# Kernel optimization log

Measured on AMD Instinct MI355X. Metric: run time of the kernel, lower is better.

## Reference

```python
import jax, jax.numpy as jnp
import numpy as np

B, T, C, H = 2, 2048, 1024, 16
D = C // H  # head_dim = 64
CH = C // 2


def _ln(x, g, b, eps=1e-5):
    m = x.mean(-1, keepdims=True)
    v = ((x - m) ** 2).mean(-1, keepdims=True)
    return (x - m) / jnp.sqrt(v + eps) * g + b


def setup_inputs() -> dict:
    key = jax.random.key(0)
    ks = iter(jax.random.split(key, 32))
    w = lambda shp: jax.random.normal(next(ks), shp, dtype=jnp.float32) * 0.02
    inp = {
        'x': jax.random.normal(next(ks), (B, T, C), dtype=jnp.float32),
        'attention_mask': jnp.ones((B, T, T), dtype=jnp.int32),
        # importance_net: Linear(C,C/2), LN(C/2), GELU, Linear(C/2,1), Sigmoid
        'imp_w1': w((C, CH)), 'imp_b1': jnp.zeros((CH,)),
        'imp_g': jnp.ones((CH,)), 'imp_beta': jnp.zeros((CH,)),
        'imp_w2': w((CH, 1)), 'imp_b2': jnp.zeros((1,)),
        # reasoning_net: Linear(C,C), LN(C), GELU, Linear(C,C)
        'rsn_w1': w((C, C)), 'rsn_b1': jnp.zeros((C,)),
        'rsn_g': jnp.ones((C,)), 'rsn_beta': jnp.zeros((C,)),
        'rsn_w2': w((C, C)), 'rsn_b2': jnp.zeros((C,)),
        # attention projections
        'q_w': w((C, C)), 'q_b': jnp.zeros((C,)),
        'k_w': w((C, C)), 'k_b': jnp.zeros((C,)),
        'v_w': w((C, C)), 'v_b': jnp.zeros((C,)),
        'o_w': w((C, C)), 'o_b': jnp.zeros((C,)),
        # temp_net: Linear(C,C/2), LN(C/2), GELU, Linear(C/2,H)
        'tmp_w1': w((C, CH)), 'tmp_b1': jnp.zeros((CH,)),
        'tmp_g': jnp.ones((CH,)), 'tmp_beta': jnp.zeros((CH,)),
        'tmp_w2': w((CH, H)), 'tmp_b2': jnp.zeros((H,)),
        # output LayerNorm
        'norm_g': jnp.ones((C,)), 'norm_b': jnp.zeros((C,)),
    }
    return inp


def reference(x, attention_mask, imp_w1, imp_b1, imp_g, imp_beta, imp_w2, imp_b2,
              rsn_w1, rsn_b1, rsn_g, rsn_beta, rsn_w2, rsn_b2,
              q_w, q_b, k_w, k_b, v_w, v_b, o_w, o_b,
              tmp_w1, tmp_b1, tmp_g, tmp_beta, tmp_w2, tmp_b2,
              norm_g, norm_b):
    Bz, Tz, Cz = x.shape
    # importance gating: [B,T,1]
    h = jax.nn.gelu(_ln(x @ imp_w1 + imp_b1, imp_g, imp_beta), approximate=False)
    importance = jnp.maximum(jax.nn.sigmoid(h @ imp_w2 + imp_b2), 1e-6)
    xi = x * importance
    # reasoning net on gated input
    h = jax.nn.gelu(_ln(xi @ rsn_w1 + rsn_b1, rsn_g, rsn_beta), approximate=False)
    reasoned = h @ rsn_w2 + rsn_b2
    # projections
    q = (reasoned @ q_w + q_b).reshape(Bz, Tz, H, D).transpose(0, 2, 1, 3)
    k = (xi @ k_w + k_b).reshape(Bz, Tz, H, D).transpose(0, 2, 1, 3)
    v = (x @ v_w + v_b).reshape(Bz, Tz, H, D).transpose(0, 2, 1, 3)
    # per-(batch,head) temperature
    ht = jax.nn.gelu(_ln(reasoned.mean(axis=1) @ tmp_w1 + tmp_b1, tmp_g, tmp_beta), approximate=False)
    temp = jax.nn.softplus(ht @ tmp_w2 + tmp_b2) + 0.5  # [B,H]
    # attention with mask and learned temperature before softmax
    scale = 1.0 / jnp.sqrt(jnp.float32(D))
    attn = jnp.einsum('bhqd,bhkd->bhqk', q, k) * scale
    attn = jnp.where(attention_mask[:, None] == 0, -jnp.inf, attn)
    attn = attn * temp[:, :, None, None]
    attn = jax.nn.softmax(attn, axis=-1)
    # dropout is identity in eval mode
    out = jnp.einsum('bhqk,bhkd->bhqd', attn, v)
    out = out.transpose(0, 2, 1, 3).reshape(Bz, Tz, Cz)
    out = out @ o_w + o_b
    return _ln(x + out, norm_g, norm_b)
```

## Files before the change

kernel.cpp:

```cpp
#include <hip/hip_runtime.h>
#include <hip/hip_bf16.h>
#include <math.h>

#define BB 2
#define TT 2048
#define CC 1024
#define HH 16
#define DD 64
#define CHALF 512
#define NN (BB * TT)
#define LOG2E 1.44269504088896340736f

typedef __attribute__((ext_vector_type(8))) short short8;
typedef __attribute__((ext_vector_type(4))) short short4_t;
typedef __attribute__((ext_vector_type(4))) float f32x4;

__device__ __forceinline__ float gelu_exact(float x) {
    return 0.5f * x * (1.0f + erff(x * 0.70710678118654752f));
}

__device__ __forceinline__ short f2bf(float f) {
    __hip_bfloat16 h = __float2bfloat16(f);
    short s;
    __builtin_memcpy(&s, &h, 2);
    return s;
}

__device__ __forceinline__ short4_t pack_bf16x4(float a, float b, float c,
                                                float d) {
    short4_t s4;
    s4[0] = f2bf(a);
    s4[1] = f2bf(b);
    s4[2] = f2bf(c);
    s4[3] = f2bf(d);
    return s4;
}

__device__ __forceinline__ void async_copy16(const void* g, void* l) {
    __builtin_amdgcn_global_load_lds(
        (const __attribute__((address_space(1))) void*)g,
        (__attribute__((address_space(3))) void*)l, 16, 0, 0);
}

__global__ __launch_bounds__(256) void prep(
    const float* __restrict__ x, __hip_bfloat16* __restrict__ x_bf,
    const int* __restrict__ mask, int* __restrict__ flags,
    const float* w0, const float* w1, const float* w2, const float* w3,
    const float* w4, const float* w5, const float* w6,
    __hip_bfloat16* t0, __hip_bfloat16* t1, __hip_bfloat16* t2,
    __hip_bfloat16* t3, __hip_bfloat16* t4, __hip_bfloat16* t5,
    __hip_bfloat16* t6) {
    __shared__ float T[64][65];
    int blk = blockIdx.x;
    int tid = threadIdx.x;
    if (blk < 2048) {
        int i = (blk * 256 + tid) * 8;
        float4 a = *(const float4*)&x[i];
        float4 b = *(const float4*)&x[i + 4];
        __hip_bfloat16 o[8] = {
            __float2bfloat16(a.x), __float2bfloat16(a.y),
            __float2bfloat16(a.z), __float2bfloat16(a.w),
            __float2bfloat16(b.x), __float2bfloat16(b.y),
            __float2bfloat16(b.z), __float2bfloat16(b.w)};
        *(float4*)&x_bf[i] = *(float4*)o;
    } else if (blk < 4096) {
        int idx = blk - 2048;
        int kt = idx & 31, qt = (idx >> 5) & 31, b = idx >> 10;
        int* red = (int*)T;
        int r = tid >> 2;
        int c0 = (tid & 3) * 16;
        const int* base =
            mask + ((size_t)(b * TT + qt * 64 + r)) * TT + kt * 64 + c0;
        int all = 1;
#pragma unroll
        for (int i = 0; i < 4; ++i) {
            int4 m4 = *(const int4*)(base + i * 4);
            all &= (m4.x != 0) & (m4.y != 0) & (m4.z != 0) & (m4.w != 0);
        }
        red[tid] = all;
        __syncthreads();
#pragma unroll
        for (int o = 128; o > 0; o >>= 1) {
            if (tid < o) red[tid] &= red[tid + o];
            __syncthreads();
        }
        if (tid == 0) flags[(b * 32 + qt) * 32 + kt] = red[0];
    } else {
        int idx = blk - 4096;
        const float* W;
        __hip_bfloat16* Wt;
        int N, n0, k0;
        if (idx < 128) {
            W = w0; Wt = t0; N = 512;
            n0 = (idx & 7) * 64;
            k0 = (idx >> 3) * 64;
        } else {
            idx -= 128;
            int w = idx >> 8;
            int r = idx & 255;
            N = 1024;
            n0 = (r & 15) * 64;
            k0 = (r >> 4) * 64;
            switch (w) {
                case 0: W = w1; Wt = t1; break;
                case 1: W = w2; Wt = t2; break;
                case 2: W = w3; Wt = t3; break;
                case 3: W = w4; Wt = t4; break;
                case 4: W = w5; Wt = t5; break;
                default: W = w6; Wt = t6; break;
            }
        }
        int c = tid & 63, r4 = tid >> 6;
#pragma unroll
        for (int i = 0; i < 16; ++i) {
            int row = i * 4 + r4;
            T[row][c] = W[(size_t)(k0 + row) * N + n0 + c];
        }
        __syncthreads();
#pragma unroll
        for (int i = 0; i < 16; ++i) {
            int row = i * 4 + r4;
            Wt[(size_t)(n0 + row) * CC + k0 + c] = __float2bfloat16(T[c][row]);
        }
    }
}

template <bool BF16OUT>
__global__ __launch_bounds__(256) void gemm_mfma64(
    const short* __restrict__ A, const short* __restrict__ Wt,
    const float* __restrict__ bias, float* __restrict__ Cf,
    __hip_bfloat16* __restrict__ Cb, int M, int N, int K) {
    __shared__ short As[64][32];
    __shared__ short Bs[128][32];
    int tid = threadIdx.x;
    int wave = tid >> 6, lane = tid & 63;
    int m16 = lane & 15, quad = lane >> 4;
    int wm = wave >> 1, wn = wave & 1;
    int row0 = blockIdx.y * 64, col0 = blockIdx.x * 128;
    int lr = lane >> 2;
    int kof = (lane & 3) * 8;

    f32x4 acc[2][4];
#pragma unroll
    for (int i = 0; i < 2; ++i)
#pragma unroll
        for (int j = 0; j < 4; ++j) acc[i][j] = (f32x4){0.f, 0.f, 0.f, 0.f};

    for (int k0 = 0; k0 < K; k0 += 32) {
        async_copy16(A + (size_t)(row0 + wave * 16 + lr) * K + k0 + kof,
                     &As[wave * 16][0]);
#pragma unroll
        for (int j = 0; j < 2; ++j) {
            int rbase = wave * 32 + j * 16;
            async_copy16(Wt + (size_t)(col0 + rbase + lr) * K + k0 + kof,
                         &Bs[rbase][0]);
        }
        __syncthreads();
        short8 af[2], bfr[4];
#pragma unroll
        for (int i = 0; i < 2; ++i)
            af[i] = *(const short8*)&As[wm * 32 + i * 16 + m16][quad * 8];
#pragma unroll
        for (int j = 0; j < 4; ++j)
            bfr[j] = *(const short8*)&Bs[wn * 64 + j * 16 + m16][quad * 8];
#pragma unroll
        for (int i = 0; i < 2; ++i)
#pragma unroll
            for (int j = 0; j < 4; ++j)
                acc[i][j] = __builtin_amdgcn_mfma_f32_16x16x32_bf16(
                    af[i], bfr[j], acc[i][j], 0, 0, 0);
        __syncthreads();
    }
#pragma unroll
    for (int i = 0; i < 2; ++i) {
#pragma unroll
        for (int j = 0; j < 4; ++j) {
            int col = col0 + wn * 64 + j * 16 + m16;
            float bv = bias[col];
#pragma unroll
            for (int rr = 0; rr < 4; ++rr) {
                int row = row0 + wm * 32 + i * 16 + quad * 4 + rr;
                float val = acc[i][j][rr] + bv;
                if (BF16OUT)
                    Cb[(size_t)row * N + col] = __float2bfloat16(val);
                else
                    Cf[(size_t)row * N + col] = val;
            }
        }
    }
}

__global__ __launch_bounds__(256) void gemm_qkv(
    const short* __restrict__ Aq, const short* __restrict__ Ak,
    const short* __restrict__ Av, const short* __restrict__ Wq,
    const short* __restrict__ Wk, const short* __restrict__ Wv,
    const float* __restrict__ bq, const float* __restrict__ bk,
    const float* __restrict__ bv, __hip_bfloat16* __restrict__ Cq,
    __hip_bfloat16* __restrict__ Ck, __hip_bfloat16* __restrict__ Cv,
    const float* __restrict__ tmp) {
    int z = blockIdx.z;
    const short* A = (z == 0) ? Aq : (z == 1) ? Ak : Av;
    const short* Wt = (z == 0) ? Wq : (z == 1) ? Wk : Wv;
    const float* bias = (z == 0) ? bq : (z == 1) ? bk : bv;

    __shared__ short As[128][32];
    __shared__ short Bs[128][32];
    int tid = threadIdx.x;
    int wave = tid >> 6, lane = tid & 63;
    int m16 = lane & 15, quad = lane >> 4;
    int wm = wave >> 1, wn = wave & 1;
    int row0 = blockIdx.y * 128, col0 = blockIdx.x * 128;
    int lr = lane >> 2;
    int kof = (lane & 3) * 8;

    float scale = 1.0f;
    if (z == 0)
        scale = tmp[(row0 >> 11) * HH + (col0 >> 6) + wn] * 0.125f * LOG2E;

    f32x4 acc[4][4];
#pragma unroll
    for (int i = 0; i < 4; ++i)
#pragma unroll
        for (int j = 0; j < 4; ++j) acc[i][j] = (f32x4){0.f, 0.f, 0.f, 0.f};

    for (int k0 = 0; k0 < CC; k0 += 32) {
#pragma unroll
        for (int j = 0; j < 2; ++j) {
            int rbase = wave * 32 + j * 16;
            async_copy16(A + (size_t)(row0 + rbase + lr) * CC + k0 + kof,
                         &As[rbase][0]);
            async_copy16(Wt + (size_t)(col0 + rbase + lr) * CC + k0 + kof,
                         &Bs[rbase][0]);
        }
        __syncthreads();
        short8 af[4], bfr[4];
#pragma unroll
        for (int i = 0; i < 4; ++i)
            af[i] = *(const short8*)&As[wm * 64 + i * 16 + m16][quad * 8];
#pragma unroll
        for (int j = 0; j < 4; ++j)
            bfr[j] = *(const short8*)&Bs[wn * 64 + j * 16 + m16][quad * 8];
#pragma unroll
        for (int i = 0; i < 4; ++i)
#pragma unroll
            for (int j = 0; j < 4; ++j)
                acc[i][j] = __builtin_amdgcn_mfma_f32_16x16x32_bf16(
                    af[i], bfr[j], acc[i][j], 0, 0, 0);
        __syncthreads();
    }
    if (z == 2) {
        int b = row0 >> 11;
        int t0r = (row0 & (TT - 1)) + wm * 64 + quad * 4;
#pragma unroll
        for (int i = 0; i < 4; ++i) {
#pragma unroll
            for (int j = 0; j < 4; ++j) {
                int col = col0 + wn * 64 + j * 16 + m16;
                int h = col >> 6, d = col & 63;
                float bv2 = bias[col];
                short4_t pk = pack_bf16x4(
                    acc[i][j][0] + bv2, acc[i][j][1] + bv2,
                    acc[i][j][2] + bv2, acc[i][j][3] + bv2);
                *(short4_t*)&Cv[(((size_t)(b * HH + h) * DD) + d) * TT + t0r +
                                i * 16] = pk;
            }
        }
    } else {
        __hip_bfloat16* C = (z == 0) ? Cq : Ck;
#pragma unroll
        for (int i = 0; i < 4; ++i) {
#pragma unroll
            for (int j = 0; j < 4; ++j) {
                int col = col0 + wn * 64 + j * 16 + m16;
                float bv2 = bias[col];
#pragma unroll
                for (int rr = 0; rr < 4; ++rr) {
                    int row = row0 + wm * 64 + i * 16 + quad * 4 + rr;
                    C[(size_t)row * CC + col] =
                        __float2bfloat16((acc[i][j][rr] + bv2) * scale);
                }
            }
        }
    }
}

__global__ __launch_bounds__(256) void imp_fused(
    const float* __restrict__ h1, const float* __restrict__ g,
    const float* __restrict__ beta, const float* __restrict__ w2,
    const float* __restrict__ b2, const float* __restrict__ x,
    __hip_bfloat16* __restrict__ xi) {
    int row = blockIdx.x;
    int tid = threadIdx.x;
    const float* hr = h1 + (size_t)row * CHALF;
    float v0 = hr[tid], v1 = hr[tid + 256];
    __shared__ float red[256];
    red[tid] = v0 + v1;
    __syncthreads();
#pragma unroll
    for (int o = 128; o > 0; o >>= 1) {
        if (tid < o) red[tid] += red[tid + o];
        __syncthreads();
    }
    float mean = red[0] * (1.0f / CHALF);
    __syncthreads();
    float d0 = v0 - mean, d1 = v1 - mean;
    red[tid] = d0 * d0 + d1 * d1;
    __syncthreads();
#pragma unroll
    for (int o = 128; o > 0; o >>= 1) {
        if (tid < o) red[tid] += red[tid + o];
        __syncthreads();
    }
    float inv = rsqrtf(red[0] * (1.0f / CHALF) + 1e-5f);
    __syncthreads();
    float ge0 = gelu_exact(d0 * inv * g[tid] + beta[tid]);
    float ge1 = gelu_exact(d1 * inv * g[tid + 256] + beta[tid + 256]);
    red[tid] = ge0 * w2[tid] + ge1 * w2[tid + 256];
    __syncthreads();
#pragma unroll
    for (int o = 128; o > 0; o >>= 1) {
        if (tid < o) red[tid] += red[tid + o];
        __syncthreads();
    }
    float z = red[0] + b2[0];
    float sg = 1.0f / (1.0f + expf(-z));
    float imp = fmaxf(sg, 1e-6f);
#pragma unroll
    for (int i = 0; i < 4; ++i) {
        int c = i * 256 + tid;
        xi[(size_t)row * CC + c] =
            __float2bfloat16(x[(size_t)row * CC + c] * imp);
    }
}

template <int WIDTH>
__global__ __launch_bounds__(256) void ln_gelu_bf16(
    const float* __restrict__ Y, const float* __restrict__ g,
    const float* __restrict__ beta, __hip_bfloat16* __restrict__ O) {
    constexpr int PT = WIDTH / 256;
    int row = blockIdx.x;
    int tid = threadIdx.x;
    const float* yr = Y + (size_t)row * WIDTH;
    float v[PT];
    float s = 0.f;
#pragma unroll
    for (int i = 0; i < PT; ++i) {
        v[i] = yr[i * 256 + tid];
        s += v[i];
    }
    __shared__ float red[256];
    red[tid] = s;
    __syncthreads();
#pragma unroll
    for (int o = 128; o > 0; o >>= 1) {
        if (tid < o) red[tid] += red[tid + o];
        __syncthreads();
    }
    float mean = red[0] * (1.0f / WIDTH);
    __syncthreads();
    s = 0.f;
#pragma unroll
    for (int i = 0; i < PT; ++i) {
        float d = v[i] - mean;
        s += d * d;
    }
    red[tid] = s;
    __syncthreads();
#pragma unroll
    for (int o = 128; o > 0; o >>= 1) {
        if (tid < o) red[tid] += red[tid + o];
        __syncthreads();
    }
    float inv = rsqrtf(red[0] * (1.0f / WIDTH) + 1e-5f);
#pragma unroll
    for (int i = 0; i < PT; ++i) {
        int c = i * 256 + tid;
        O[(size_t)row * WIDTH + c] =
            __float2bfloat16(gelu_exact((v[i] - mean) * inv * g[c] + beta[c]));
    }
}

__global__ __launch_bounds__(256) void mean_part(
    const __hip_bfloat16* __restrict__ R, float* __restrict__ part) {
    int idx = blockIdx.x * 256 + threadIdx.x;
    int c = idx & (CC - 1);
    int chunk = (idx >> 10) & 15;
    int b = idx >> 14;
    const __hip_bfloat16* base = R + ((size_t)(b * TT + chunk * 128)) * CC + c;
    float s = 0.f;
    for (int t = 0; t < 128; ++t) s += __bfloat162float(base[(size_t)t * CC]);
    part[idx] = s;
}

__global__ __launch_bounds__(256) void temp_gemv1(
    const float* __restrict__ part, const float* __restrict__ w1,
    const float* __restrict__ b1, float* __restrict__ acc1) {
    __shared__ float rm_l[CC];
    __shared__ float red[256];
    int b = blockIdx.y;
    int c0 = blockIdx.x * 64;
    int tid = threadIdx.x;
    for (int cc = tid; cc < CC; cc += 256) {
        float s = 0.f;
#pragma unroll
        for (int ch = 0; ch < 16; ++ch)
            s += part[(size_t)(b * 16 + ch) * CC + cc];
        rm_l[cc] = s * (1.0f / TT);
    }
    __syncthreads();
    int col = c0 + (tid & 63);
    int kq = tid >> 6;
    float s = 0.f;
#pragma unroll 8
    for (int i = kq * 256; i < kq * 256 + 256; ++i)
        s = fmaf(rm_l[i], w1[(size_t)i * CHALF + col], s);
    red[tid] = s;
    __syncthreads();
    if (tid < 64) {
        float t = red[tid] + red[tid + 64] + red[tid + 128] + red[tid + 192];
        acc1[b * CHALF + tid + c0] = t + b1[col];
    }
}

__global__ __launch_bounds__(512) void temp_fin(
    const float* __restrict__ acc1, const float* __restrict__ g,
    const float* __restrict__ beta, const float* __restrict__ w2,
    const float* __restrict__ b2, float* __restrict__ temp) {
    __shared__ float red[512];
    __shared__ float wred[8][16];
    int b = blockIdx.x;
    int tid = threadIdx.x;
    int wave = tid >> 6, lane = tid & 63;
    float acc = acc1[b * CHALF + tid];
    red[tid] = acc;
    __syncthreads();
#pragma unroll
    for (int o = 256; o > 0; o >>= 1) {
        if (tid < o) red[tid] += red[tid + o];
        __syncthreads();
    }
    float mean = red[0] * (1.0f / CHALF);
    __syncthreads();
    float d = acc - mean;
    red[tid] = d * d;
    __syncthreads();
#pragma unroll
    for (int o = 256; o > 0; o >>= 1) {
        if (tid < o) red[tid] += red[tid + o];
        __syncthreads();
    }
    float inv = rsqrtf(red[0] * (1.0f / CHALF) + 1e-5f);
    float ht = gelu_exact((acc - mean) * inv * g[tid] + beta[tid]);
    float p[16];
#pragma unroll
    for (int j = 0; j < 16; ++j) p[j] = ht * w2[tid * HH + j];
#pragma unroll
    for (int off = 1; off < 64; off <<= 1)
#pragma unroll
        for (int j = 0; j < 16; ++j) p[j] += __shfl_xor(p[j], off, 64);
    if (lane == 0)
#pragma unroll
        for (int j = 0; j < 16; ++j) wred[wave][j] = p[j];
    __syncthreads();
    if (tid < HH) {
        float s = b2[tid];
#pragma unroll
        for (int w = 0; w < 8; ++w) s += wred[w][tid];
        float sp = fmaxf(s, 0.f) + log1pf(expf(-fabsf(s)));
        temp[b * HH + tid] = sp + 0.5f;
    }
}

__global__ __launch_bounds__(256) void flash_attn_mfma(
    const short* __restrict__ q, const short* __restrict__ k,
    const short* __restrict__ vt, const int* __restrict__ mask,
    const int* __restrict__ flags, __hip_bfloat16* __restrict__ out) {
    __shared__ short Ks[64][72];
    __shared__ short Vt[64][72];
    __shared__ short Ps[128][72];
    int tid = threadIdx.x;
    int wave = tid >> 6, lane = tid & 63;
    int m16 = lane & 15, quad = lane >> 4;
    int qt = blockIdx.x;
    int q0 = qt * 128;
    int bh = blockIdx.y;
    int b = bh >> 4, h = bh & 15;

    short8 qf[2][2];
#pragma unroll
    for (int qg = 0; qg < 2; ++qg) {
        const short* qrow = q + ((size_t)(b * TT + q0 + wave * 32 + qg * 16 + m16)) * CC +
                            h * DD + quad * 8;
        qf[qg][0] = *(const short8*)(qrow);
        qf[qg][1] = *(const short8*)(qrow + 32);
    }

    float m_run[2] = {-INFINITY, -INFINITY};
    float l_run[2] = {0.f, 0.f};
    f32x4 acc_o[2][4];
#pragma unroll
    for (int qg = 0; qg < 2; ++qg)
#pragma unroll
        for (int t = 0; t < 4; ++t) acc_o[qg][t] = (f32x4){0.f, 0.f, 0.f, 0.f};

    for (int kt = 0; kt < TT / 64; ++kt) {
        int kb = kt * 64;
#pragma unroll
        for (int i = 0; i < 2; ++i) {
            int idx = i * 256 + tid;
            int r = idx >> 3;
            int dc = (idx & 7) * 8;
            *(short8*)&Ks[r][dc] =
                *(const short8*)(k + ((size_t)(b * TT + kb + r)) * CC + h * DD + dc);
            *(short8*)&Vt[r][dc] =
                *(const short8*)(vt + ((size_t)bh * DD + r) * TT + kb + dc);
        }
        __syncthreads();

        short8 kf[4][2];
#pragma unroll
        for (int t = 0; t < 4; ++t) {
            kf[t][0] = *(const short8*)&Ks[t * 16 + m16][quad * 8];
            kf[t][1] = *(const short8*)&Ks[t * 16 + m16][32 + quad * 8];
        }
        int fl = flags[(b * 32 + 2 * qt + (wave >> 1)) * 32 + kt];

#pragma unroll
        for (int qg = 0; qg < 2; ++qg) {
            f32x4 sacc[4];
#pragma unroll
            for (int t = 0; t < 4; ++t) sacc[t] = (f32x4){0.f, 0.f, 0.f, 0.f};
#pragma unroll
            for (int t = 0; t < 4; ++t) {
                sacc[t] = __builtin_amdgcn_mfma_f32_16x16x32_bf16(kf[t][0], qf[qg][0], sacc[t], 0, 0, 0);
                sacc[t] = __builtin_amdgcn_mfma_f32_16x16x32_bf16(kf[t][1], qf[qg][1], sacc[t], 0, 0, 0);
            }
            float sv[4][4];
#pragma unroll
            for (int t = 0; t < 4; ++t)
#pragma unroll
                for (int r = 0; r < 4; ++r) sv[t][r] = sacc[t][r];
            if (fl == 0) {
                int qrow = q0 + wave * 32 + qg * 16 + m16;
#pragma unroll
                for (int t = 0; t < 4; ++t)
#pragma unroll
                    for (int r = 0; r < 4; ++r) {
                        int kg = kb + t * 16 + quad * 4 + r;
                        if (mask[((size_t)(b * TT + qrow)) * TT + kg] == 0)
                            sv[t][r] = -INFINITY;
                    }
            }
            float mx = sv[0][0];
#pragma unroll
            for (int t = 0; t < 4; ++t)
#pragma unroll
                for (int r = 0; r < 4; ++r) mx = fmaxf(mx, sv[t][r]);
            mx = fmaxf(mx, __shfl_xor(mx, 16, 64));
            mx = fmaxf(mx, __shfl_xor(mx, 32, 64));
            float mnew = fmaxf(m_run[qg], mx);
            float alpha = __builtin_amdgcn_exp2f(m_run[qg] - mnew);
            m_run[qg] = mnew;
            int prow = wave * 32 + qg * 16 + m16;
            float psum = 0.f;
#pragma unroll
            for (int t = 0; t < 4; ++t) {
                short4_t pk;
#pragma unroll
                for (int r = 0; r < 4; ++r) {
                    float p = __builtin_amdgcn_exp2f(sv[t][r] - mnew);
                    psum += p;
                    pk[r] = f2bf(p);
                }
                *(short4_t*)&Ps[prow][t * 16 + quad * 4] = pk;
            }
            psum += __shfl_xor(psum, 16, 64);
            psum += __shfl_xor(psum, 32, 64);
            l_run[qg] = l_run[qg] * alpha + psum;
#pragma unroll
            for (int r = 0; r < 4; ++r) {
                float ar = __shfl(alpha, (lane & 48) | (quad * 4 + r), 64);
#pragma unroll
                for (int td = 0; td < 4; ++td) acc_o[qg][td][r] *= ar;
            }
        }

#pragma unroll
        for (int kc = 0; kc < 2; ++kc) {
            short8 vf[4];
#pragma unroll
            for (int td = 0; td < 4; ++td)
                vf[td] = *(const short8*)&Vt[td * 16 + m16][kc * 32 + quad * 8];
#pragma unroll
            for (int qg = 0; qg < 2; ++qg) {
                short8 pf = *(const short8*)&Ps[wave * 32 + qg * 16 + m16][kc * 32 + quad * 8];
#pragma unroll
                for (int td = 0; td < 4; ++td)
                    acc_o[qg][td] = __builtin_amdgcn_mfma_f32_16x16x32_bf16(
                        pf, vf[td], acc_o[qg][td], 0, 0, 0);
            }
        }
        __syncthreads();
    }

#pragma unroll
    for (int qg = 0; qg < 2; ++qg) {
#pragma unroll
        for (int r = 0; r < 4; ++r) {
            float lr = __shfl(l_run[qg], (lane & 48) | (quad * 4 + r), 64);
            float inv = 1.0f / lr;
            int row = b * TT + q0 + wave * 32 + qg * 16 + quad * 4 + r;
#pragma unroll
            for (int td = 0; td < 4; ++td)
                out[(size_t)row * CC + h * DD + td * 16 + m16] =
                    __float2bfloat16(acc_o[qg][td][r] * inv);
        }
    }
}

__global__ __launch_bounds__(256) void final_ln(
    const float* __restrict__ x, const float* __restrict__ p,
    const float* __restrict__ g, const float* __restrict__ beta,
    float* __restrict__ out) {
    int row = blockIdx.x;
    int tid = threadIdx.x;
    const float* xr = x + (size_t)row * CC;
    const float* pr = p + (size_t)row * CC;
    float v[4];
    float s = 0.f;
#pragma unroll
    for (int i = 0; i < 4; ++i) {
        int c = i * 256 + tid;
        v[i] = xr[c] + pr[c];
        s += v[i];
    }
    __shared__ float red[256];
    red[tid] = s;
    __syncthreads();
#pragma unroll
    for (int o = 128; o > 0; o >>= 1) {
        if (tid < o) red[tid] += red[tid + o];
        __syncthreads();
    }
    float mean = red[0] * (1.0f / CC);
    __syncthreads();
    s = 0.f;
#pragma unroll
    for (int i = 0; i < 4; ++i) {
        float d = v[i] - mean;
        s += d * d;
    }
    red[tid] = s;
    __syncthreads();
#pragma unroll
    for (int o = 128; o > 0; o >>= 1) {
        if (tid < o) red[tid] += red[tid + o];
        __syncthreads();
    }
    float inv = rsqrtf(red[0] * (1.0f / CC) + 1e-5f);
#pragma unroll
    for (int i = 0; i < 4; ++i) {
        int c = i * 256 + tid;
        out[(size_t)row * CC + c] = (v[i] - mean) * inv * g[c] + beta[c];
    }
}

extern "C" void kernel_launch(void* const* d_in, const int* in_sizes, int n_in,
                              void* d_out, int out_size, void* d_ws,
                              size_t ws_size, hipStream_t stream) {
    const float* x        = (const float*)d_in[0];
    const int*   mask     = (const int*)d_in[1];
    const float* imp_w1   = (const float*)d_in[2];
    const float* imp_b1   = (const float*)d_in[3];
    const float* imp_g    = (const float*)d_in[4];
    const float* imp_beta = (const float*)d_in[5];
    const float* imp_w2   = (const float*)d_in[6];
    const float* imp_b2   = (const float*)d_in[7];
    const float* rsn_w1   = (const float*)d_in[8];
    const float* rsn_b1   = (const float*)d_in[9];
    const float* rsn_g    = (const float*)d_in[10];
    const float* rsn_beta = (const float*)d_in[11];
    const float* rsn_w2   = (const float*)d_in[12];
    const float* rsn_b2   = (const float*)d_in[13];
    const float* q_w      = (const float*)d_in[14];
    const float* q_b      = (const float*)d_in[15];
    const float* k_w      = (const float*)d_in[16];
    const float* k_b      = (const float*)d_in[17];
    const float* v_w      = (const float*)d_in[18];
    const float* v_b      = (const float*)d_in[19];
    const float* o_w      = (const float*)d_in[20];
    const float* o_b      = (const float*)d_in[21];
    const float* tmp_w1   = (const float*)d_in[22];
    const float* tmp_b1   = (const float*)d_in[23];
    const float* tmp_g    = (const float*)d_in[24];
    const float* tmp_beta = (const float*)d_in[25];
    const float* tmp_w2   = (const float*)d_in[26];
    const float* tmp_b2   = (const float*)d_in[27];
    const float* norm_g   = (const float*)d_in[28];
    const float* norm_b   = (const float*)d_in[29];
    float* out = (float*)d_out;
    float* ws  = (float*)d_ws;

    float* h1  = ws;
    float* h2  = ws + 2097152;
    __hip_bfloat16* x_bf  = (__hip_bfloat16*)(ws + 6291456);
    __hip_bfloat16* xi_bf = (__hip_bfloat16*)(ws + 8388608);
    __hip_bfloat16* h2b   = (__hip_bfloat16*)(ws + 10485760);
    __hip_bfloat16* rs_bf = (__hip_bfloat16*)(ws + 12582912);
    __hip_bfloat16* qb    = (__hip_bfloat16*)(ws + 14680064);
    __hip_bfloat16* kb    = (__hip_bfloat16*)(ws + 16777216);
    __hip_bfloat16* vtb   = (__hip_bfloat16*)(ws + 20971520);
    __hip_bfloat16* imp_w1t = (__hip_bfloat16*)(ws + 23068672);
    __hip_bfloat16* rsn_w1t = (__hip_bfloat16*)(ws + 23330816);
    __hip_bfloat16* rsn_w2t = (__hip_bfloat16*)(ws + 23855104);
    __hip_bfloat16* q_wt    = (__hip_bfloat16*)(ws + 24379392);
    __hip_bfloat16* k_wt    = (__hip_bfloat16*)(ws + 24903680);
    __hip_bfloat16* v_wt    = (__hip_bfloat16*)(ws + 25427968);
    __hip_bfloat16* o_wt    = (__hip_bfloat16*)(ws + 25952256);
    float* tmp  = ws + 26478592;
    float* part = ws + 26479104;
    int*   flg  = (int*)(ws + 26511872);
    float* acc1 = ws + 26513920;

    dim3 blk(256);
    prep<<<5760, blk, 0, stream>>>(
        x, x_bf, mask, flg,
        imp_w1, rsn_w1, rsn_w2, q_w, k_w, v_w, o_w,
        imp_w1t, rsn_w1t, rsn_w2t, q_wt, k_wt, v_wt, o_wt);

    gemm_mfma64<false><<<dim3(CHALF / 128, NN / 64), blk, 0, stream>>>(
        (const short*)x_bf, (const short*)imp_w1t, imp_b1, h1, nullptr, NN, CHALF, CC);
    imp_fused<<<NN, blk, 0, stream>>>(h1, imp_g, imp_beta, imp_w2, imp_b2, x, xi_bf);
    gemm_mfma64<false><<<dim3(CC / 128, NN / 64), blk, 0, stream>>>(
        (const short*)xi_bf, (const short*)rsn_w1t, rsn_b1, h2, nullptr, NN, CC, CC);
    ln_gelu_bf16<CC><<<NN, blk, 0, stream>>>(h2, rsn_g, rsn_beta, h2b);
    gemm_mfma64<true><<<dim3(CC / 128, NN / 64), blk, 0, stream>>>(
        (const short*)h2b, (const short*)rsn_w2t, rsn_b2, nullptr, rs_bf, NN, CC, CC);
    mean_part<<<128, blk, 0, stream>>>(rs_bf, part);
    temp_gemv1<<<dim3(CHALF / 64, BB), blk, 0, stream>>>(part, tmp_w1, tmp_b1, acc1);
    temp_fin<<<BB, dim3(512), 0, stream>>>(acc1, tmp_g, tmp_beta, tmp_w2, tmp_b2, tmp);
    gemm_qkv<<<dim3(CC / 128, NN / 128, 3), blk, 0, stream>>>(
        (const short*)rs_bf, (const short*)xi_bf, (const short*)x_bf,
        (const short*)q_wt, (const short*)k_wt, (const short*)v_wt,
        q_b, k_b, v_b, qb, kb, vtb, tmp);
    flash_attn_mfma<<<dim3(TT / 128, BB * HH), blk, 0, stream>>>(
        (const short*)qb, (const short*)kb, (const short*)vtb, mask, flg, rs_bf);
    gemm_mfma64<false><<<dim3(CC / 128, NN / 64), blk, 0, stream>>>(
        (const short*)rs_bf, (const short*)o_wt, o_b, h2, nullptr, NN, CC, CC);
    final_ln<<<NN, blk, 0, stream>>>(x, h2, norm_g, norm_b, out);
}
```

Measured before the change: 424.5 us.

## Widen GEMM k-step, add lazy flash rescale, transpose PV output layout

The projection GEMM now loads two 32-wide k-slices per barrier pair, halving synchronization per k. In the attention kernel the P·V MFMA operands are swapped, so each lane holds four contiguous d-values of one query row. That removes the per-row alpha/l shuffles and allows packed 8-byte bf16 stores. The online-softmax rescale is also skipped when no row max increases. The wave-uniform __any branch adds divergence-free control flow, and the GEMM uses twice the LDS.

Result: faster. 413.9 us (-2.5%).

```diff
diff --git a/kernel.cpp b/kernel.cpp
--- a/kernel.cpp
+++ b/kernel.cpp
@@ -130,8 +130,8 @@
     const short* __restrict__ A, const short* __restrict__ Wt,
     const float* __restrict__ bias, float* __restrict__ Cf,
     __hip_bfloat16* __restrict__ Cb, int M, int N, int K) {
-    __shared__ short As[64][32];
-    __shared__ short Bs[128][32];
+    __shared__ short As0[64][32], As1[64][32];
+    __shared__ short Bs0[128][32], Bs1[128][32];
     int tid = threadIdx.x;
     int wave = tid >> 6, lane = tid & 63;
     int m16 = lane & 15, quad = lane >> 4;
@@ -146,29 +146,37 @@
 #pragma unroll
         for (int j = 0; j < 4; ++j) acc[i][j] = (f32x4){0.f, 0.f, 0.f, 0.f};
 
-    for (int k0 = 0; k0 < K; k0 += 32) {
-        async_copy16(A + (size_t)(row0 + wave * 16 + lr) * K + k0 + kof,
-                     &As[wave * 16][0]);
+    for (int k0 = 0; k0 < K; k0 += 64) {
+        const short* arow = A + (size_t)(row0 + wave * 16 + lr) * K + k0 + kof;
+        async_copy16(arow, &As0[wave * 16][0]);
+        async_copy16(arow + 32, &As1[wave * 16][0]);
 #pragma unroll
         for (int j = 0; j < 2; ++j) {
             int rbase = wave * 32 + j * 16;
-            async_copy16(Wt + (size_t)(col0 + rbase + lr) * K + k0 + kof,
-                         &Bs[rbase][0]);
-        }
-        __syncthreads();
-        short8 af[2], bfr[4];
-#pragma unroll
-        for (int i = 0; i < 2; ++i)
-            af[i] = *(const short8*)&As[wm * 32 + i * 16 + m16][quad * 8];
-#pragma unroll
-        for (int j = 0; j < 4; ++j)
-            bfr[j] = *(const short8*)&Bs[wn * 64 + j * 16 + m16][quad * 8];
-#pragma unroll
-        for (int i = 0; i < 2; ++i)
+            const short* brow =
+                Wt + (size_t)(col0 + rbase + lr) * K + k0 + kof;
+            async_copy16(brow, &Bs0[rbase][0]);
+            async_copy16(brow + 32, &Bs1[rbase][0]);
+        }
+        __syncthreads();
+#pragma unroll
+        for (int kc = 0; kc < 2; ++kc) {
+            short8 af[2], bfr[4];
+#pragma unroll
+            for (int i = 0; i < 2; ++i)
+                af[i] = kc ? *(const short8*)&As1[wm * 32 + i * 16 + m16][quad * 8]
+                           : *(const short8*)&As0[wm * 32 + i * 16 + m16][quad * 8];
 #pragma unroll
             for (int j = 0; j < 4; ++j)
-                acc[i][j] = __builtin_amdgcn_mfma_f32_16x16x32_bf16(
-                    af[i], bfr[j], acc[i][j], 0, 0, 0);
+                bfr[j] = kc ? *(const short8*)&Bs1[wn * 64 + j * 16 + m16][quad * 8]
+                            : *(const short8*)&Bs0[wn * 64 + j * 16 + m16][quad * 8];
+#pragma unroll
+            for (int i = 0; i < 2; ++i)
+#pragma unroll
+                for (int j = 0; j < 4; ++j)
+                    acc[i][j] = __builtin_amdgcn_mfma_f32_16x16x32_bf16(
+                        af[i], bfr[j], acc[i][j], 0, 0, 0);
+        }
         __syncthreads();
     }
 #pragma unroll
@@ -559,7 +567,14 @@
             mx = fmaxf(mx, __shfl_xor(mx, 16, 64));
             mx = fmaxf(mx, __shfl_xor(mx, 32, 64));
             float mnew = fmaxf(m_run[qg], mx);
-            float alpha = __builtin_amdgcn_exp2f(m_run[qg] - mnew);
+            if (__any(mnew > m_run[qg])) {
+                float alpha = __builtin_amdgcn_exp2f(m_run[qg] - mnew);
+                l_run[qg] *= alpha;
+#pragma unroll
+                for (int td = 0; td < 4; ++td)
+#pragma unroll
+                    for (int r = 0; r < 4; ++r) acc_o[qg][td][r] *= alpha;
+            }
             m_run[qg] = mnew;
             int prow = wave * 32 + qg * 16 + m16;
             float psum = 0.f;
@@ -576,13 +591,7 @@
             }
             psum += __shfl_xor(psum, 16, 64);
             psum += __shfl_xor(psum, 32, 64);
-            l_run[qg] = l_run[qg] * alpha + psum;
-#pragma unroll
-            for (int r = 0; r < 4; ++r) {
-                float ar = __shfl(alpha, (lane & 48) | (quad * 4 + r), 64);
-#pragma unroll
-                for (int td = 0; td < 4; ++td) acc_o[qg][td][r] *= ar;
-            }
+            l_run[qg] += psum;
         }
 
 #pragma unroll
@@ -597,7 +606,7 @@
 #pragma unroll
                 for (int td = 0; td < 4; ++td)
                     acc_o[qg][td] = __builtin_amdgcn_mfma_f32_16x16x32_bf16(
-                        pf, vf[td], acc_o[qg][td], 0, 0, 0);
+                        vf[td], pf, acc_o[qg][td], 0, 0, 0);
             }
         }
         __syncthreads();
@@ -605,15 +614,14 @@
 
 #pragma unroll
     for (int qg = 0; qg < 2; ++qg) {
-#pragma unroll
-        for (int r = 0; r < 4; ++r) {
-            float lr = __shfl(l_run[qg], (lane & 48) | (quad * 4 + r), 64);
-            float inv = 1.0f / lr;
-            int row = b * TT + q0 + wave * 32 + qg * 16 + quad * 4 + r;
-#pragma unroll
-            for (int td = 0; td < 4; ++td)
-                out[(size_t)row * CC + h * DD + td * 16 + m16] =
-                    __float2bfloat16(acc_o[qg][td][r] * inv);
+        float inv = 1.0f / l_run[qg];
+        int row = b * TT + q0 + wave * 32 + qg * 16 + m16;
+#pragma unroll
+        for (int td = 0; td < 4; ++td) {
+            short4_t pk = pack_bf16x4(
+                acc_o[qg][td][0] * inv, acc_o[qg][td][1] * inv,
+                acc_o[qg][td][2] * inv, acc_o[qg][td][3] * inv);
+            *(short4_t*)&out[(size_t)row * CC + h * DD + td * 16 + quad * 4] = pk;
         }
     }
 }
```
